# Kernel optimization log

Hardware: AMD Instinct MI355X
Metric: run time of the kernel (lower is better)

Reference implementation:

```python
import jax, jax.numpy as jnp
import numpy as np

# truncation bit counts per layer (from Net __init__ kwargs); relu uses n=0 (no-op)
N_CONV1 = 13
N_CONV2 = 13
N_FC1 = 13
N_FC2 = 13
HIDDEN = 500
BATCH = 4096


def trunc(x, n):
    """Zero out the low n bits of the float32 mantissa (bitwise, like numpy round-trip in torch code)."""
    if n == 0:
        return x
    b = jax.lax.bitcast_convert_type(x, jnp.int32) & np.int32(-1 << n)
    return jax.lax.bitcast_convert_type(b, jnp.float32)


def conv2d(x, w, b):
    # NCHW / OIHW, stride 1, VALID padding (padding=0 in torch module)
    y = jax.lax.conv_general_dilated(x, w, window_strides=(1, 1), padding='VALID',
                                     dimension_numbers=('NCHW', 'OIHW', 'NCHW'))
    return y + b[None, :, None, None]


def max_pool_2x2(x):
    return jax.lax.reduce_window(x, -jnp.inf, jax.lax.max,
                                 window_dimensions=(1, 1, 2, 2),
                                 window_strides=(1, 1, 2, 2), padding='VALID')


def setup_inputs() -> dict:
    key = jax.random.key(0)
    ks = jax.random.split(key, 9)
    x = jax.random.normal(ks[0], (BATCH, 1, 28, 28), dtype=jnp.float32)
    # kaiming-uniform-ish init scales (fan_in based)
    def u(k, shape, fan_in):
        bound = 1.0 / np.sqrt(fan_in)
        return jax.random.uniform(k, shape, jnp.float32, -bound, bound)
    w_conv1 = u(ks[1], (20, 1, 5, 5), 1 * 25)
    b_conv1 = u(ks[2], (20,), 1 * 25)
    w_conv2 = u(ks[3], (50, 20, 5, 5), 20 * 25)
    b_conv2 = u(ks[4], (50,), 20 * 25)
    w_fc1 = u(ks[5], (HIDDEN, 800), 800)
    b_fc1 = u(ks[6], (HIDDEN,), 800)
    w_fc2 = u(ks[7], (10, HIDDEN), HIDDEN)
    b_fc2 = u(ks[8], (10,), HIDDEN)
    return {"x": x, "w_conv1": w_conv1, "b_conv1": b_conv1,
            "w_conv2": w_conv2, "b_conv2": b_conv2,
            "w_fc1": w_fc1, "b_fc1": b_fc1,
            "w_fc2": w_fc2, "b_fc2": b_fc2}


def reference(x, w_conv1, b_conv1, w_conv2, b_conv2, w_fc1, b_fc1, w_fc2, b_fc2):
    # conv1 -> trunc -> relu (relu n=0, so plain relu)
    h = jnp.maximum(trunc(conv2d(x, w_conv1, b_conv1), N_CONV1), 0.0)   # [B,20,24,24]
    h = max_pool_2x2(h)                                                  # [B,20,12,12]
    h = jnp.maximum(trunc(conv2d(h, w_conv2, b_conv2), N_CONV2), 0.0)   # [B,50,8,8]
    h = max_pool_2x2(h)                                                  # [B,50,4,4]
    h = h.reshape(-1, 4 * 4 * 50)                                        # [B,800]
    h = jnp.maximum(trunc(h @ w_fc1.T + b_fc1[None, :], N_FC1), 0.0)    # [B,HIDDEN]
    h = trunc(h @ w_fc2.T + b_fc2[None, :], N_FC2)                       # [B,10]
    return jax.nn.log_softmax(h, axis=1)
```

## Files before the change

### kernel.cpp

```cpp
#include <hip/hip_runtime.h>


typedef _Float16 v8h __attribute__((ext_vector_type(8)));
typedef float v4f __attribute__((ext_vector_type(4)));

__device__ __forceinline__ float trunc13(float v) {
    return __int_as_float(__float_as_int(v) & (int)0xFFFFE000u);
}

__global__ void k_prep(const float* __restrict__ w1, const float* __restrict__ w2,
                       const float* __restrict__ wf1,
                       _Float16* __restrict__ wpc1, _Float16* __restrict__ wph,
                       _Float16* __restrict__ wpf1) {
    int id = blockIdx.x * 256 + threadIdx.x;
    if (id < 1280) {
        int t = id >> 6, oc = id & 63;
        _Float16* dh = wph + (size_t)id * 32;
        for (int s = 0; s < 32; ++s) {
            int k = t * 32 + s;
            int pix = (k * 2731) >> 16;
            int icr = k - pix * 24;
            float w = 0.f;
            if (pix < 25 && icr < 20 && oc < 50)
                w = w2[oc * 500 + icr * 25 + pix];
            dh[s] = (_Float16)w;
        }
    } else if (id < 1408) {
        int l = id - 1280;
        int lane = l & 63, tile = l >> 6;
        int rr = lane & 15, kg = lane >> 4;
        int oc = tile * 16 + rr;
        _Float16* dst = wpc1 + (size_t)l * 8;
        for (int j = 0; j < 8; ++j) {
            int t = kg * 8 + j;
            float w = (oc < 20 && t < 25) ? w1[oc * 25 + t] : 0.f;
            dst[j] = (_Float16)w;
        }
    } else if (id < 14208) {
        int id2 = id - 1408;
        int t = id2 >> 9, oc = id2 & 511;
        _Float16* dst = wpf1 + (size_t)id2 * 64;
        for (int kk = 0; kk < 32; ++kk) {
            float w = (oc < 500) ? wf1[(size_t)oc * 800 + t * 32 + kk] : 0.f;
            _Float16 hi = (_Float16)w;
            dst[kk] = hi;
            dst[32 + kk] = (_Float16)(w - (float)hi);
        }
    }
}

__global__ __launch_bounds__(256) void k_conv1(const float* __restrict__ x,
                                               const _Float16* __restrict__ wpc1,
                                               const float* __restrict__ b1,
                                               _Float16* __restrict__ p1h) {
    int tid = threadIdx.x;
    int wid = tid >> 6, lane = tid & 63;
    int b = blockIdx.x * 4 + wid;
    int kg = lane >> 4, rr = lane & 15;
    int py = rr >> 2, px = rr & 3;

    v8h bf0 = *(const v8h*)(wpc1 + (size_t)lane * 8);
    v8h bf1 = *(const v8h*)(wpc1 + (size_t)(64 + lane) * 8);
    float bias0 = b1[rr];
    float bias1 = (rr < 4) ? b1[16 + rr] : 0.f;

    int off[8];
#pragma unroll
    for (int j = 0; j < 8; ++j) {
        int t = kg * 8 + j;
        if (t > 24) t = 24;
        int ky = (t * 205) >> 10;
        int kx = t - 5 * ky;
        off[j] = (py + ky) * 28 + (px + kx);
    }

    const float* img = x + (size_t)b * 784;
    _Float16* outb = p1h + (size_t)b * 144 * 24;

    for (int qy = 0; qy < 6; ++qy) {
#pragma unroll
        for (int qx = 0; qx < 6; ++qx) {
            const float* base = img + (qy * 4) * 28 + qx * 4;
            v8h a;
#pragma unroll
            for (int j = 0; j < 8; ++j) a[j] = (_Float16)base[off[j]];

            v4f acc0 = {0.f, 0.f, 0.f, 0.f}, acc1 = {0.f, 0.f, 0.f, 0.f};
            acc0 = __builtin_amdgcn_mfma_f32_16x16x32_f16(a, bf0, acc0, 0, 0, 0);
            acc1 = __builtin_amdgcn_mfma_f32_16x16x32_f16(a, bf1, acc1, 0, 0, 0);

            float z0 = fmaxf(trunc13(acc0[0] + bias0), 0.f);
            float z1 = fmaxf(trunc13(acc0[1] + bias0), 0.f);
            float z2 = fmaxf(trunc13(acc0[2] + bias0), 0.f);
            float z3 = fmaxf(trunc13(acc0[3] + bias0), 0.f);
            float m01 = fmaxf(z0, z1), m23 = fmaxf(z2, z3);
            float p01 = fmaxf(m01, __shfl_xor(m01, 16, 64));
            float p23 = fmaxf(m23, __shfl_xor(m23, 16, 64));
            float y0 = fmaxf(trunc13(acc1[0] + bias1), 0.f);
            float y1 = fmaxf(trunc13(acc1[1] + bias1), 0.f);
            float y2 = fmaxf(trunc13(acc1[2] + bias1), 0.f);
            float y3 = fmaxf(trunc13(acc1[3] + bias1), 0.f);
            float n01 = fmaxf(y0, y1), n23 = fmaxf(y2, y3);
            float q01 = fmaxf(n01, __shfl_xor(n01, 16, 64));
            float q23 = fmaxf(n23, __shfl_xor(n23, 16, 64));

            if (!(kg & 1)) {
                int pos0 = (2 * qy + (kg >> 1)) * 12 + 2 * qx;
                _Float16* o = outb + (size_t)pos0 * 24;
                o[rr]      = (_Float16)p01;
                o[24 + rr] = (_Float16)p23;
                if (rr < 4) {
                    o[16 + rr]      = (_Float16)q01;
                    o[24 + 16 + rr] = (_Float16)q23;
                }
            }
        }
    }
}

#define AIMG3 3744
__global__ __launch_bounds__(256, 2) void k_conv2(const _Float16* __restrict__ p1h,
                                                  const _Float16* __restrict__ wph,
                                                  const float* __restrict__ b2,
                                                  _Float16* __restrict__ p2h) {
    __shared__ __align__(16) _Float16 Al[8 * AIMG3];
    int tid = threadIdx.x;
    int b0 = blockIdx.x * 8;

    {
        const uint4* src = (const uint4*)(p1h + (size_t)b0 * 3456);
        uint4* dst = (uint4*)Al;
        uint4 z = make_uint4(0u, 0u, 0u, 0u);
        for (int i = tid; i < 3744; i += 256) {
            int img = i / 468, r = i - img * 468;
            dst[i] = (r < 432) ? src[img * 432 + r] : z;
        }
    }
    __syncthreads();

    int wid = tid >> 6, lane = tid & 63;
    int kg = lane >> 4, rr = lane & 15;
    int Y = rr >> 3, xx = rr & 7;
    const _Float16* Ab0 = Al + (wid * 2) * AIMG3;
    const _Float16* Ab1 = Ab0 + AIMG3;
    const _Float16* abase[8];
#pragma unroll
    for (int my = 0; my < 4; ++my) {
        abase[my]     = Ab0 + ((2 * my + Y) * 12 + xx) * 24;
        abase[my + 4] = Ab1 + ((2 * my + Y) * 12 + xx) * 24;
    }
    const _Float16* bh_base = wph + rr * 32 + kg * 8;

    v4f acc[8][4];
#pragma unroll
    for (int my = 0; my < 8; ++my)
#pragma unroll
        for (int nt = 0; nt < 4; ++nt) acc[my][nt] = (v4f){0.f, 0.f, 0.f, 0.f};

    for (int u = 0; u < 10; ++u) {
        int t0 = 2 * u, t1 = 2 * u + 1;
        v8h bA[4], bB[4];
#pragma unroll
        for (int nt = 0; nt < 4; ++nt) {
            bA[nt] = *(const v8h*)(bh_base + t0 * 2048 + nt * 512);
            bB[nt] = *(const v8h*)(bh_base + t1 * 2048 + nt * 512);
        }
        {
            int k0 = t0 * 32 + kg * 8;
            int pix = (k0 * 2731) >> 16;
            int icol = k0 - pix * 24;
            int ky = (pix * 205) >> 10;
            int kx = pix - 5 * ky;
            int aofs = (ky * 12 + kx) * 24 + icol;
            v8h af[8];
#pragma unroll
            for (int my = 0; my < 8; ++my)
                af[my] = *(const v8h*)(abase[my] + aofs);
#pragma unroll
            for (int my = 0; my < 8; ++my)
#pragma unroll
                for (int nt = 0; nt < 4; ++nt)
                    acc[my][nt] = __builtin_amdgcn_mfma_f32_16x16x32_f16(af[my], bA[nt], acc[my][nt], 0, 0, 0);
        }
        {
            int k0 = t1 * 32 + kg * 8;
            int pix = (k0 * 2731) >> 16;
            int icol = k0 - pix * 24;
            int ky = (pix * 205) >> 10;
            int kx = pix - 5 * ky;
            int aofs = (ky * 12 + kx) * 24 + icol;
            v8h af[8];
#pragma unroll
            for (int my = 0; my < 8; ++my)
                af[my] = *(const v8h*)(abase[my] + aofs);
#pragma unroll
            for (int my = 0; my < 8; ++my)
#pragma unroll
                for (int nt = 0; nt < 4; ++nt)
                    acc[my][nt] = __builtin_amdgcn_mfma_f32_16x16x32_f16(af[my], bB[nt], acc[my][nt], 0, 0, 0);
        }
    }

#pragma unroll
    for (int h = 0; h < 2; ++h) {
        int imgg = b0 + wid * 2 + h;
#pragma unroll
        for (int nt = 0; nt < 4; ++nt) {
            int oc = nt * 16 + rr;
            float bias = (oc < 50) ? b2[oc] : 0.f;
#pragma unroll
            for (int my = 0; my < 4; ++my) {
                v4f a = acc[h * 4 + my][nt];
                float z0 = fmaxf(trunc13(a[0] + bias), 0.f);
                float z1 = fmaxf(trunc13(a[1] + bias), 0.f);
                float z2 = fmaxf(trunc13(a[2] + bias), 0.f);
                float z3 = fmaxf(trunc13(a[3] + bias), 0.f);
                float s0 = fmaxf(z0, z1), s2 = fmaxf(z2, z3);
                float o0 = fmaxf(s0, __shfl_xor(s0, 32, 64));
                float o2 = fmaxf(s2, __shfl_xor(s2, 32, 64));
                if (kg < 2 && oc < 50) {
                    p2h[(size_t)imgg * 800 + oc * 16 + my * 4 + 2 * kg]     = (_Float16)o0;
                    p2h[(size_t)imgg * 800 + oc * 16 + my * 4 + 2 * kg + 1] = (_Float16)o2;
                }
            }
        }
    }
}

__global__ __launch_bounds__(256) void k_fc1(const _Float16* __restrict__ Ah,
                                             const _Float16* __restrict__ Bp,
                                             const float* __restrict__ bias,
                                             _Float16* __restrict__ Hh) {
    __shared__ _Float16 Al[2][4096];
    __shared__ _Float16 Bl[2][2560];
    int tid = threadIdx.x;
    int i0 = blockIdx.x * 128, n0 = blockIdx.y * 64;
    int wid = tid >> 6, lane = tid & 63;
    int rr = lane & 15, kg = lane >> 4;

    int ca0 = tid, ca1 = tid + 256;
    int ra0_ = ca0 >> 2, qa0 = ca0 & 3, ra1_ = ca1 >> 2, qa1 = ca1 & 3;
    int aw0 = (ra0_ * 4 + (qa0 ^ ((ra0_ >> 1) & 3))) * 8;
    int aw1 = (ra1_ * 4 + (qa1 ^ ((ra1_ >> 1) & 3))) * 8;
    int bwB = ((tid >> 2) * 5 + (tid & 3)) * 8;

    uint4 xa0, xa1, xb0;
    auto loadT = [&](int t) {
        xa0 = *(const uint4*)(Ah + (size_t)(i0 + ra0_) * 800 + t * 32 + qa0 * 8);
        xa1 = *(const uint4*)(Ah + (size_t)(i0 + ra1_) * 800 + t * 32 + qa1 * 8);
        const uint4* g = (const uint4*)Bp + (size_t)t * 4096 + (size_t)n0 * 8;
        xb0 = g[(tid >> 2) * 8 + (tid & 3)];
    };
    auto writeT = [&](int buf) {
        *(uint4*)(&Al[buf][aw0]) = xa0;
        *(uint4*)(&Al[buf][aw1]) = xa1;
        *(uint4*)(&Bl[buf][bwB]) = xb0;
    };

    int aoff[2], bhoff[4];
#pragma unroll
    for (int mf = 0; mf < 2; ++mf) {
        int r = wid * 32 + mf * 16 + rr;
        aoff[mf] = (r * 4 + (kg ^ ((rr >> 1) & 3))) * 8;
    }
#pragma unroll
    for (int nf = 0; nf < 4; ++nf)
        bhoff[nf] = ((nf * 16 + rr) * 5 + kg) * 8;

    v4f zero = {0.f, 0.f, 0.f, 0.f};
    v4f acc[2][4];
#pragma unroll
    for (int mf = 0; mf < 2; ++mf)
#pragma unroll
        for (int nf = 0; nf < 4; ++nf) acc[mf][nf] = zero;

    loadT(0);
    writeT(0);
    __syncthreads();

    for (int t = 0; t < 25; ++t) {
        int cur = t & 1;
        if (t < 24) loadT(t + 1);
        v8h af[2], bh[4];
#pragma unroll
        for (int mf = 0; mf < 2; ++mf) af[mf] = *(const v8h*)(&Al[cur][aoff[mf]]);
#pragma unroll
        for (int nf = 0; nf < 4; ++nf) bh[nf] = *(const v8h*)(&Bl[cur][bhoff[nf]]);
#pragma unroll
        for (int mf = 0; mf < 2; ++mf)
#pragma unroll
            for (int nf = 0; nf < 4; ++nf)
                acc[mf][nf] = __builtin_amdgcn_mfma_f32_16x16x32_f16(af[mf], bh[nf], acc[mf][nf], 0, 0, 0);
        if (t < 24) writeT(cur ^ 1);
        __syncthreads();
    }

#pragma unroll
    for (int mf = 0; mf < 2; ++mf)
#pragma unroll
        for (int nf = 0; nf < 4; ++nf) {
            int col = n0 + nf * 16 + rr;
            float bs = bias[col < 500 ? col : 0];
#pragma unroll
            for (int j = 0; j < 4; ++j) {
                int row = i0 + wid * 32 + mf * 16 + kg * 4 + j;
                float v = fmaxf(trunc13(acc[mf][nf][j] + bs), 0.f);
                if (col < 500) Hh[(size_t)row * 512 + col] = (_Float16)v;
            }
        }
}

__global__ __launch_bounds__(256) void k_fc2(const _Float16* __restrict__ Hh,
                                             const float* __restrict__ W,
                                             const float* __restrict__ bias,
                                             float* __restrict__ out) {
    int wave = threadIdx.x >> 6;
    int lane = threadIdx.x & 63;
    int i = blockIdx.x * 4 + wave;
    const _Float16* hrow = Hh + (size_t)i * 512;

    float p[10];
#pragma unroll
    for (int j = 0; j < 10; ++j) p[j] = 0.f;
    for (int k = lane; k < 500; k += 64) {
        float h = (float)hrow[k];
#pragma unroll
        for (int j = 0; j < 10; ++j) p[j] += h * W[j * 500 + k];
    }
#pragma unroll
    for (int j = 0; j < 10; ++j)
#pragma unroll
        for (int off = 32; off; off >>= 1) p[j] += __shfl_xor(p[j], off, 64);

    if (lane == 0) {
        float z[10], m = -1e30f;
#pragma unroll
        for (int j = 0; j < 10; ++j) {
            z[j] = trunc13(p[j] + bias[j]);
            m = fmaxf(m, z[j]);
        }
        float s = 0.f;
#pragma unroll
        for (int j = 0; j < 10; ++j) s += expf(z[j] - m);
        float lse = m + logf(s);
#pragma unroll
        for (int j = 0; j < 10; ++j) out[(size_t)i * 10 + j] = z[j] - lse;
    }
}

extern "C" void kernel_launch(void* const* d_in, const int* in_sizes, int n_in,
                              void* d_out, int out_size, void* d_ws, size_t ws_size,
                              hipStream_t stream) {
    const float* x   = (const float*)d_in[0];
    const float* w1  = (const float*)d_in[1];
    const float* b1  = (const float*)d_in[2];
    const float* w2  = (const float*)d_in[3];
    const float* b2  = (const float*)d_in[4];
    const float* wf1 = (const float*)d_in[5];
    const float* bf1 = (const float*)d_in[6];
    const float* wf2 = (const float*)d_in[7];
    const float* bf2 = (const float*)d_in[8];
    float* out = (float*)d_out;

    char* ws = (char*)d_ws;
    _Float16* p1h  = (_Float16*)(ws);
    _Float16* p2h  = (_Float16*)(ws + 28311552);
    _Float16* h1h  = (_Float16*)(ws + 34865152);
    _Float16* wph  = (_Float16*)(ws + 39059456);
    _Float16* wpf1 = (_Float16*)(ws + 39141376);
    _Float16* wpc1 = (_Float16*)(ws + 40779776);

    k_prep<<<56, 256, 0, stream>>>(w1, w2, wf1, wpc1, wph, wpf1);
    k_conv1<<<1024, 256, 0, stream>>>(x, wpc1, b1, p1h);
    k_conv2<<<512, 256, 0, stream>>>(p1h, wph, b2, p2h);
    dim3 g3(32, 8);
    k_fc1<<<g3, 256, 0, stream>>>(p2h, wpf1, bf1, h1h);
    k_fc2<<<1024, 256, 0, stream>>>(h1h, wf2, bf2, out);
}
```

Measured before the change: 96.89 us.

## Trim padded conv2 K-steps and read fc1 operands straight from global memory

The conv2 MFMA loop now runs 19 K-tiles of 32 instead of 20. K=600 (25 pixels × 24 padded channels) fits in 19 tiles, so the last all-zero padded tile is skipped. The fc1 GEMM drops its LDS double buffering and __syncthreads, and each lane loads its A and B fragments directly from global memory, relying on L1/L2 caching. This removes barrier and LDS traffic but adds redundant global loads across waves, with less latency hiding.

```diff
diff --git a/kernel.cpp b/kernel.cpp
--- a/kernel.cpp
+++ b/kernel.cpp
@@ -157,7 +157,27 @@
 #pragma unroll
         for (int nt = 0; nt < 4; ++nt) acc[my][nt] = (v4f){0.f, 0.f, 0.f, 0.f};
 
-    for (int u = 0; u < 10; ++u) {
+#define CSTEP(T, BV)                                                          \
+    {                                                                         \
+        int k0 = (T) * 32 + kg * 8;                                           \
+        int pix = (k0 * 2731) >> 16;                                          \
+        int icol = k0 - pix * 24;                                             \
+        int ky = (pix * 205) >> 10;                                           \
+        int kx = pix - 5 * ky;                                                \
+        int aofs = (ky * 12 + kx) * 24 + icol;                                \
+        v8h af[8];                                                            \
+        _Pragma("unroll")                                                     \
+        for (int my = 0; my < 8; ++my)                                        \
+            af[my] = *(const v8h*)(abase[my] + aofs);                         \
+        _Pragma("unroll")                                                     \
+        for (int my = 0; my < 8; ++my)                                        \
+            _Pragma("unroll")                                                 \
+            for (int nt = 0; nt < 4; ++nt)                                    \
+                acc[my][nt] = __builtin_amdgcn_mfma_f32_16x16x32_f16(         \
+                    af[my], BV[nt], acc[my][nt], 0, 0, 0);                    \
+    }
+
+    for (int u = 0; u < 9; ++u) {
         int t0 = 2 * u, t1 = 2 * u + 1;
         v8h bA[4], bB[4];
 #pragma unroll
@@ -165,41 +185,17 @@
             bA[nt] = *(const v8h*)(bh_base + t0 * 2048 + nt * 512);
             bB[nt] = *(const v8h*)(bh_base + t1 * 2048 + nt * 512);
         }
-        {
-            int k0 = t0 * 32 + kg * 8;
-            int pix = (k0 * 2731) >> 16;
-            int icol = k0 - pix * 24;
-            int ky = (pix * 205) >> 10;
-            int kx = pix - 5 * ky;
-            int aofs = (ky * 12 + kx) * 24 + icol;
-            v8h af[8];
-#pragma unroll
-            for (int my = 0; my < 8; ++my)
-                af[my] = *(const v8h*)(abase[my] + aofs);
-#pragma unroll
-            for (int my = 0; my < 8; ++my)
-#pragma unroll
-                for (int nt = 0; nt < 4; ++nt)
-                    acc[my][nt] = __builtin_amdgcn_mfma_f32_16x16x32_f16(af[my], bA[nt], acc[my][nt], 0, 0, 0);
-        }
-        {
-            int k0 = t1 * 32 + kg * 8;
-            int pix = (k0 * 2731) >> 16;
-            int icol = k0 - pix * 24;
-            int ky = (pix * 205) >> 10;
-            int kx = pix - 5 * ky;
-            int aofs = (ky * 12 + kx) * 24 + icol;
-            v8h af[8];
-#pragma unroll
-            for (int my = 0; my < 8; ++my)
-                af[my] = *(const v8h*)(abase[my] + aofs);
-#pragma unroll
-            for (int my = 0; my < 8; ++my)
-#pragma unroll
-                for (int nt = 0; nt < 4; ++nt)
-                    acc[my][nt] = __builtin_amdgcn_mfma_f32_16x16x32_f16(af[my], bB[nt], acc[my][nt], 0, 0, 0);
-        }
-    }
+        CSTEP(t0, bA);
+        CSTEP(t1, bB);
+    }
+    {
+        v8h bA[4];
+#pragma unroll
+        for (int nt = 0; nt < 4; ++nt)
+            bA[nt] = *(const v8h*)(bh_base + 18 * 2048 + nt * 512);
+        CSTEP(18, bA);
+    }
+#undef CSTEP
 
 #pragma unroll
     for (int h = 0; h < 2; ++h) {
@@ -231,68 +227,39 @@
                                              const _Float16* __restrict__ Bp,
                                              const float* __restrict__ bias,
                                              _Float16* __restrict__ Hh) {
-    __shared__ _Float16 Al[2][4096];
-    __shared__ _Float16 Bl[2][2560];
     int tid = threadIdx.x;
     int i0 = blockIdx.x * 128, n0 = blockIdx.y * 64;
     int wid = tid >> 6, lane = tid & 63;
     int rr = lane & 15, kg = lane >> 4;
 
-    int ca0 = tid, ca1 = tid + 256;
-    int ra0_ = ca0 >> 2, qa0 = ca0 & 3, ra1_ = ca1 >> 2, qa1 = ca1 & 3;
-    int aw0 = (ra0_ * 4 + (qa0 ^ ((ra0_ >> 1) & 3))) * 8;
-    int aw1 = (ra1_ * 4 + (qa1 ^ ((ra1_ >> 1) & 3))) * 8;
-    int bwB = ((tid >> 2) * 5 + (tid & 3)) * 8;
-
-    uint4 xa0, xa1, xb0;
-    auto loadT = [&](int t) {
-        xa0 = *(const uint4*)(Ah + (size_t)(i0 + ra0_) * 800 + t * 32 + qa0 * 8);
-        xa1 = *(const uint4*)(Ah + (size_t)(i0 + ra1_) * 800 + t * 32 + qa1 * 8);
-        const uint4* g = (const uint4*)Bp + (size_t)t * 4096 + (size_t)n0 * 8;
-        xb0 = g[(tid >> 2) * 8 + (tid & 3)];
-    };
-    auto writeT = [&](int buf) {
-        *(uint4*)(&Al[buf][aw0]) = xa0;
-        *(uint4*)(&Al[buf][aw1]) = xa1;
-        *(uint4*)(&Bl[buf][bwB]) = xb0;
-    };
-
-    int aoff[2], bhoff[4];
-#pragma unroll
-    for (int mf = 0; mf < 2; ++mf) {
-        int r = wid * 32 + mf * 16 + rr;
-        aoff[mf] = (r * 4 + (kg ^ ((rr >> 1) & 3))) * 8;
-    }
+    const _Float16* arow[2];
+#pragma unroll
+    for (int mf = 0; mf < 2; ++mf)
+        arow[mf] = Ah + (size_t)(i0 + wid * 32 + mf * 16 + rr) * 800 + kg * 8;
+    const _Float16* brow[4];
 #pragma unroll
     for (int nf = 0; nf < 4; ++nf)
-        bhoff[nf] = ((nf * 16 + rr) * 5 + kg) * 8;
-
-    v4f zero = {0.f, 0.f, 0.f, 0.f};
+        brow[nf] = Bp + (size_t)(n0 + nf * 16 + rr) * 64 + kg * 8;
+
     v4f acc[2][4];
 #pragma unroll
     for (int mf = 0; mf < 2; ++mf)
 #pragma unroll
-        for (int nf = 0; nf < 4; ++nf) acc[mf][nf] = zero;
-
-    loadT(0);
-    writeT(0);
-    __syncthreads();
+        for (int nf = 0; nf < 4; ++nf) acc[mf][nf] = (v4f){0.f, 0.f, 0.f, 0.f};
 
     for (int t = 0; t < 25; ++t) {
-        int cur = t & 1;
-        if (t < 24) loadT(t + 1);
         v8h af[2], bh[4];
 #pragma unroll
-        for (int mf = 0; mf < 2; ++mf) af[mf] = *(const v8h*)(&Al[cur][aoff[mf]]);
-#pragma unroll
-        for (int nf = 0; nf < 4; ++nf) bh[nf] = *(const v8h*)(&Bl[cur][bhoff[nf]]);
+        for (int mf = 0; mf < 2; ++mf)
+            af[mf] = *(const v8h*)(arow[mf] + t * 32);
+#pragma unroll
+        for (int nf = 0; nf < 4; ++nf)
+            bh[nf] = *(const v8h*)(brow[nf] + (size_t)t * 32768);
 #pragma unroll
         for (int mf = 0; mf < 2; ++mf)
 #pragma unroll
             for (int nf = 0; nf < 4; ++nf)
                 acc[mf][nf] = __builtin_amdgcn_mfma_f32_16x16x32_f16(af[mf], bh[nf], acc[mf][nf], 0, 0, 0);
-        if (t < 24) writeT(cur ^ 1);
-        __syncthreads();
     }
 
 #pragma unroll
```

Result: slower. 100.5 us (+3.7%).
